# Kernel optimization log

Measured on AMD Instinct MI355X. Metric: run time of the kernel, lower is better.

The kernel has to match this reference:

```python
import jax, jax.numpy as jnp
import numpy as np


def setup_inputs() -> dict:
    key = jax.random.key(0)
    k1, k2, k3 = jax.random.split(key, 3)
    B, Tc, Tq, D = 8, 4096, 1024, 256
    context = jax.random.normal(k1, (B, Tc, D), dtype=jnp.float32)
    question = jax.random.normal(k2, (B, Tq, D), dtype=jnp.float32)
    w = jax.random.normal(k3, (3 * D, 1), dtype=jnp.float32) * 0.05
    return {"context": context, "question": question, "w": w}


def reference(context, question, w):
    # context: (B, Tc, D); question: (B, Tq, D); w: (3D, 1)
    D = context.shape[-1]
    w1, w2, w3 = w[:D, 0], w[D:2 * D, 0], w[2 * D:, 0]
    # Fused similarity: S[b,i,j] = w1.c_i + w2.q_j + w3.(c_i*q_j)
    # (mathematically identical to the tiled concat + linear score, but
    # avoids materializing the (B,Tc,Tq,3D) tensor)
    s_c = jnp.einsum('bid,d->bi', context, w1)              # (B, Tc)
    s_q = jnp.einsum('bjd,d->bj', question, w2)             # (B, Tq)
    s_cq = jnp.einsum('bid,bjd->bij', context * w3, question)  # (B, Tc, Tq)
    S = s_cq + s_c[:, :, None] + s_q[:, None, :]
    A = jax.nn.softmax(S, axis=-1)                           # (B, Tc, Tq)
    # C2Q attention: U[b,i] = sum_j A[b,i,j] * q_j
    U = jnp.einsum('bij,bjd->bid', A, question)              # (B, Tc, D)
    # Q2C attention: b_i = max_j A[b,i,j]; h = sum_i b_i * c_i, tiled over Tc
    b = jnp.max(A, axis=-1)                                  # (B, Tc)
    h = jnp.einsum('bi,bid->bd', b, context)                 # (B, D)
    H = jnp.broadcast_to(h[:, None, :], context.shape)       # (B, Tc, D)
    # megamerge
    G = jnp.concatenate([context, U, context * U, context * H], axis=-1)
    return G  # (B, Tc, 4D)
```

## Files before the change

kernel.cpp:

```cpp
#include <hip/hip_runtime.h>
#include <hip/hip_bf16.h>
#include <stdint.h>
#include <stddef.h>


#define NB 8
#define TC 4096
#define TQ 1024
#define DD 256
#define JT 32
#define NJT (TQ / JT)

typedef __attribute__((ext_vector_type(4)))  float  f32x4v;
typedef __attribute__((ext_vector_type(8)))  __bf16 bf16x8v;
typedef __attribute__((ext_vector_type(4)))  __bf16 bf16x4v;

#define QA_OFF   0
#define QX_OFF   (QA_OFF + NB*NJT*16*1024)
#define SQ_OFF   (QX_OFF + NB*NJT*16*1024)
#define HV_OFF   (SQ_OFF + NB*TQ*4)

__global__ __launch_bounds__(256) void k_qprep(const float* __restrict__ question,
                                               const float* __restrict__ w,
                                               char* __restrict__ ws) {
  uint4* qa = (uint4*)(ws + QA_OFF);
  uint4* qx = (uint4*)(ws + QX_OFF);
  float* sq = (float*)(ws + SQ_OFF);
  __shared__ __align__(16) __bf16 T[32][264];

  int bx = blockIdx.x;
  int b = bx >> 5, it = bx & 31;
  int t = threadIdx.x;
  int j = t >> 3;
  int seg = t & 7;

  const float* qrow = question + ((size_t)(b * TQ + it * JT + j)) * DD + seg * 32;
  const float* w2 = w + DD;

  float part = 0.f;
#pragma unroll
  for (int k = 0; k < 8; ++k) {
    float4 v  = *(const float4*)(qrow + 4 * k);
    float4 wv = *(const float4*)(w2 + seg * 32 + 4 * k);
    part += v.x * wv.x + v.y * wv.y + v.z * wv.z + v.w * wv.w;
    bf16x4v pk = {(__bf16)v.x, (__bf16)v.y, (__bf16)v.z, (__bf16)v.w};
    *(bf16x4v*)&T[j][seg * 32 + 4 * k] = pk;
  }
  part += __shfl_xor(part, 1);
  part += __shfl_xor(part, 2);
  part += __shfl_xor(part, 4);
  if (seg == 0) sq[b * TQ + it * JT + j] = part;
  __syncthreads();

#pragma unroll
  for (int p = 0; p < 4; ++p) {
    int ch = t + 256 * p;
    int L = ch & 63, cc = ch >> 6;
    int jm = cc >> 3, c = cc & 7;
    int nh = L & 15, qh = L >> 4;
    uint4 v = *(const uint4*)&T[16 * jm + nh][32 * c + 8 * qh];
    qa[(size_t)(b * NJT + it) * 1024 + ch] = v;
  }
#pragma unroll
  for (int p = 0; p < 4; ++p) {
    int ch = t + 256 * p;
    int L = ch & 63, mt = ch >> 6;
    int nh = L & 15, qh = L >> 4;
    __bf16 e[8];
#pragma unroll
    for (int o = 0; o < 8; ++o) e[o] = T[8 * qh + o][16 * mt + nh];
    qx[(size_t)(b * NJT + it) * 1024 + ch] = *(const uint4*)e;
  }
}

__global__ __launch_bounds__(256, 2) void k_main(const float* __restrict__ context,
                                                 const float* __restrict__ w,
                                                 const char* __restrict__ ws,
                                                 float* __restrict__ hv,
                                                 float* __restrict__ out) {
  const uint4*  qa = (const uint4*)(ws + QA_OFF);
  const __bf16* qx = (const __bf16*)(ws + QX_OFF);
  const float*  sq = (const float*)(ws + SQ_OFF);

  __shared__ __align__(16) __bf16 pa_lds[2][4][16][40];
  __shared__ __align__(16) float  sq_all[TQ];
  __shared__ __align__(16) float  red_lm[2][4][16][2];
  __shared__ __align__(16) float  rinv_lds[64];
  __shared__ __align__(16) float  bvv_lds[64];

  int bx = blockIdx.x;
  int b = bx & 7;
  int ig = bx >> 3;
  int t = threadIdx.x;
  int wv = t >> 6;
  int lane = t & 63;
  int wi = wv >> 1;
  int wj = wv & 1;
  int it0 = 2 * wi, it1 = 2 * wi + 1;
  int nh = lane & 15;
  int qh = lane >> 4;

  const uint4* qa_b = qa + (size_t)b * NJT * 1024;
  const __bf16* qx_b = qx + (size_t)b * NJT * 8192;
  const float* sqb = sq + b * TQ;

  const uint4* qa_w = qa_b + (size_t)wj * 512 + lane;

  bf16x8v cw3f0[8], cw3f1[8];
  {
    const float* crow0 = context + ((size_t)(b * TC + ig * 64 + 32 * wi + nh)) * DD;
    const float* crow1 = crow0 + 16 * DD;
    const float* w3 = w + 2 * DD;
#pragma unroll
    for (int c = 0; c < 8; ++c) {
      int d0 = 32 * c + 8 * qh;
      float4 g0 = *(const float4*)(w3 + d0);
      float4 g1 = *(const float4*)(w3 + d0 + 4);
      float4 f0 = *(const float4*)(crow0 + d0);
      float4 f1 = *(const float4*)(crow0 + d0 + 4);
      bf16x8v fr;
      fr[0] = (__bf16)(f0.x * g0.x); fr[1] = (__bf16)(f0.y * g0.y);
      fr[2] = (__bf16)(f0.z * g0.z); fr[3] = (__bf16)(f0.w * g0.w);
      fr[4] = (__bf16)(f1.x * g1.x); fr[5] = (__bf16)(f1.y * g1.y);
      fr[6] = (__bf16)(f1.z * g1.z); fr[7] = (__bf16)(f1.w * g1.w);
      cw3f0[c] = fr;
      float4 h0 = *(const float4*)(crow1 + d0);
      float4 h1 = *(const float4*)(crow1 + d0 + 4);
      bf16x8v hr;
      hr[0] = (__bf16)(h0.x * g0.x); hr[1] = (__bf16)(h0.y * g0.y);
      hr[2] = (__bf16)(h0.z * g0.z); hr[3] = (__bf16)(h0.w * g0.w);
      hr[4] = (__bf16)(h1.x * g1.x); hr[5] = (__bf16)(h1.y * g1.y);
      hr[6] = (__bf16)(h1.z * g1.z); hr[7] = (__bf16)(h1.w * g1.w);
      cw3f1[c] = hr;
    }
  }

  ((float4*)sq_all)[t] = ((const float4*)sqb)[t];

  bf16x8v afr[8];
#pragma unroll
  for (int c = 0; c < 8; ++c) afr[c] = *(const bf16x8v*)(qa_w + c * 64);

  f32x4v U[16];
#pragma unroll
  for (int k = 0; k < 16; ++k) U[k] = (f32x4v){0.f, 0.f, 0.f, 0.f};
  float m0_run = -1e30f, l0_run = 0.f;
  float m1_run = -1e30f, l1_run = 0.f;

  __syncthreads();

  {
    f32x4v S0 = {0.f, 0.f, 0.f, 0.f}, S1 = {0.f, 0.f, 0.f, 0.f};
#pragma unroll
    for (int c = 0; c < 8; ++c) {
      S0 = __builtin_amdgcn_mfma_f32_16x16x32_bf16(afr[c], cw3f0[c], S0, 0, 0, 0);
      S1 = __builtin_amdgcn_mfma_f32_16x16x32_bf16(afr[c], cw3f1[c], S1, 0, 0, 0);
    }
#pragma unroll
    for (int c = 0; c < 8; ++c) afr[c] = *(const bf16x8v*)(qa_w + 1024 + c * 64);

    float4 sqv = *(const float4*)&sq_all[16 * wj + 4 * qh];
    float a0 = S0[0] + sqv.x, a1 = S0[1] + sqv.y, a2 = S0[2] + sqv.z, a3 = S0[3] + sqv.w;
    float b0 = S1[0] + sqv.x, b1 = S1[1] + sqv.y, b2 = S1[2] + sqv.z, b3 = S1[3] + sqv.w;
    float e0 = __expf(a0), e1 = __expf(a1), e2 = __expf(a2), e3 = __expf(a3);
    float f0 = __expf(b0), f1 = __expf(b1), f2 = __expf(b2), f3 = __expf(b3);
    m0_run = fmaxf(m0_run, fmaxf(fmaxf(a0, a1), fmaxf(a2, a3)));
    m1_run = fmaxf(m1_run, fmaxf(fmaxf(b0, b1), fmaxf(b2, b3)));
    l0_run += (e0 + e1) + (e2 + e3);
    l1_run += (f0 + f1) + (f2 + f3);
    bf16x4v pk0 = {(__bf16)e0, (__bf16)e1, (__bf16)e2, (__bf16)e3};
    bf16x4v pk1 = {(__bf16)f0, (__bf16)f1, (__bf16)f2, (__bf16)f3};
    *(bf16x4v*)&pa_lds[0][it0][nh][16 * wj + 4 * qh] = pk0;
    *(bf16x4v*)&pa_lds[0][it1][nh][16 * wj + 4 * qh] = pk1;
    asm volatile("s_waitcnt lgkmcnt(0)\n\ts_barrier" ::: "memory");
  }

  for (int itq = 1; itq < NJT; ++itq) {
    int cur = itq & 1;

    bf16x8v bqr[4];
    {
      const __bf16* qxt = qx_b + (size_t)(itq - 1) * 8192 + lane * 8;
#pragma unroll
      for (int nt = 0; nt < 4; ++nt)
        bqr[nt] = *(const bf16x8v*)(qxt + (size_t)(wv * 4 + nt) * 512);
    }

    f32x4v S0 = {0.f, 0.f, 0.f, 0.f}, S1 = {0.f, 0.f, 0.f, 0.f};
#pragma unroll
    for (int c = 0; c < 8; ++c) {
      S0 = __builtin_amdgcn_mfma_f32_16x16x32_bf16(afr[c], cw3f0[c], S0, 0, 0, 0);
      S1 = __builtin_amdgcn_mfma_f32_16x16x32_bf16(afr[c], cw3f1[c], S1, 0, 0, 0);
    }

    if (itq + 1 < NJT) {
#pragma unroll
      for (int c = 0; c < 8; ++c)
        afr[c] = *(const bf16x8v*)(qa_w + (size_t)(itq + 1) * 1024 + c * 64);
    }

#pragma unroll
    for (int mi = 0; mi < 4; ++mi) {
      bf16x8v af = *(const bf16x8v*)&pa_lds[cur ^ 1][mi][nh][8 * qh];
#pragma unroll
      for (int nt = 0; nt < 4; ++nt)
        U[mi * 4 + nt] = __builtin_amdgcn_mfma_f32_16x16x32_bf16(af, bqr[nt], U[mi * 4 + nt], 0, 0, 0);
    }

    float4 sqv = *(const float4*)&sq_all[itq * JT + 16 * wj + 4 * qh];
    float a0 = S0[0] + sqv.x, a1 = S0[1] + sqv.y, a2 = S0[2] + sqv.z, a3 = S0[3] + sqv.w;
    float b0 = S1[0] + sqv.x, b1 = S1[1] + sqv.y, b2 = S1[2] + sqv.z, b3 = S1[3] + sqv.w;
    float e0 = __expf(a0), e1 = __expf(a1), e2 = __expf(a2), e3 = __expf(a3);
    float f0 = __expf(b0), f1 = __expf(b1), f2 = __expf(b2), f3 = __expf(b3);
    m0_run = fmaxf(m0_run, fmaxf(fmaxf(a0, a1), fmaxf(a2, a3)));
    m1_run = fmaxf(m1_run, fmaxf(fmaxf(b0, b1), fmaxf(b2, b3)));
    l0_run += (e0 + e1) + (e2 + e3);
    l1_run += (f0 + f1) + (f2 + f3);

    bf16x4v pk0 = {(__bf16)e0, (__bf16)e1, (__bf16)e2, (__bf16)e3};
    bf16x4v pk1 = {(__bf16)f0, (__bf16)f1, (__bf16)f2, (__bf16)f3};
    *(bf16x4v*)&pa_lds[cur][it0][nh][16 * wj + 4 * qh] = pk0;
    *(bf16x4v*)&pa_lds[cur][it1][nh][16 * wj + 4 * qh] = pk1;

    asm volatile("s_waitcnt lgkmcnt(0)\n\ts_barrier" ::: "memory");
  }

  {
    bf16x8v bqr[4];
    const __bf16* qxt = qx_b + (size_t)(NJT - 1) * 8192 + lane * 8;
#pragma unroll
    for (int nt = 0; nt < 4; ++nt)
      bqr[nt] = *(const bf16x8v*)(qxt + (size_t)(wv * 4 + nt) * 512);
#pragma unroll
    for (int mi = 0; mi < 4; ++mi) {
      bf16x8v af = *(const bf16x8v*)&pa_lds[(NJT - 1) & 1][mi][nh][8 * qh];
#pragma unroll
      for (int nt = 0; nt < 4; ++nt)
        U[mi * 4 + nt] = __builtin_amdgcn_mfma_f32_16x16x32_bf16(af, bqr[nt], U[mi * 4 + nt], 0, 0, 0);
    }
  }

  float lo0 = l0_run + __shfl_xor(l0_run, 16); lo0 += __shfl_xor(lo0, 32);
  float lo1 = l1_run + __shfl_xor(l1_run, 16); lo1 += __shfl_xor(lo1, 32);
  float mo0 = fmaxf(m0_run, __shfl_xor(m0_run, 16)); mo0 = fmaxf(mo0, __shfl_xor(mo0, 32));
  float mo1 = fmaxf(m1_run, __shfl_xor(m1_run, 16)); mo1 = fmaxf(mo1, __shfl_xor(mo1, 32));
  if (lane < 16) {
    red_lm[wj][it0][nh][0] = lo0; red_lm[wj][it0][nh][1] = mo0;
    red_lm[wj][it1][nh][0] = lo1; red_lm[wj][it1][nh][1] = mo1;
  }
  __syncthreads();
  if (t < 64) {
    int it = t >> 4, n = t & 15;
    float l = red_lm[0][it][n][0] + red_lm[1][it][n][0];
    float m = fmaxf(red_lm[0][it][n][1], red_lm[1][it][n][1]);
    float ri = 1.0f / l;
    rinv_lds[t] = ri;
    bvv_lds[t] = __expf(m) * ri;
  }
  __syncthreads();

  float hacc[4] = {0.f, 0.f, 0.f, 0.f};
#pragma unroll
  for (int mi = 0; mi < 4; ++mi) {
#pragma unroll
    for (int r = 0; r < 4; ++r) {
      int rl = mi * 16 + 4 * qh + r;
      int row = ig * 64 + rl;
      float rv = rinv_lds[rl];
      float bb = bvv_lds[rl];
      const float* crow = context + ((size_t)(b * TC + row)) * DD;
      float* orow = out + ((size_t)(b * TC + row)) * (4 * DD);
#pragma unroll
      for (int nt = 0; nt < 4; ++nt) {
        int d = wv * 64 + nt * 16 + nh;
        float c = crow[d];
        float u = U[mi * 4 + nt][r] * rv;
        orow[d] = c;
        orow[DD + d] = u;
        orow[2 * DD + d] = c * u;
        hacc[nt] += bb * c;
      }
    }
  }
#pragma unroll
  for (int nt = 0; nt < 4; ++nt) {
    float h = hacc[nt] + __shfl_xor(hacc[nt], 16);
    h += __shfl_xor(h, 32);
    if (qh == 0) atomicAdd(&hv[b * DD + wv * 64 + nt * 16 + nh], h);
  }
}

__global__ __launch_bounds__(256) void k_final(const float* __restrict__ context,
                                               const char* __restrict__ ws,
                                               float* __restrict__ out) {
  const float* hv = (const float*)(ws + HV_OFF);
  int gid = blockIdx.x * 256 + threadIdx.x;
  int row = gid >> 6;
  int d = (gid & 63) * 4;
  int b = row >> 12;
  float4 c4 = ((const float4*)context)[gid];
  float4 h4 = *(const float4*)(hv + b * DD + d);
  float4 r;
  r.x = c4.x * h4.x; r.y = c4.y * h4.y; r.z = c4.z * h4.z; r.w = c4.w * h4.w;
  *(float4*)(out + (size_t)row * TQ + 3 * DD + d) = r;
}

extern "C" void kernel_launch(void* const* d_in, const int* in_sizes, int n_in,
                              void* d_out, int out_size, void* d_ws, size_t ws_size,
                              hipStream_t stream) {
  (void)in_sizes; (void)n_in; (void)out_size; (void)ws_size;
  const float* context  = (const float*)d_in[0];
  const float* question = (const float*)d_in[1];
  const float* w        = (const float*)d_in[2];
  float* out = (float*)d_out;
  char* ws = (char*)d_ws;

  k_qprep<<<NB * NJT, 256, 0, stream>>>(question, w, ws);
  hipMemsetAsync(ws + HV_OFF, 0, NB * DD * sizeof(float), stream);
  k_main<<<NB * (TC / 64), 256, 0, stream>>>(context, w, ws,
                                             (float*)(ws + HV_OFF), out);
  k_final<<<(NB * TC * DD / 4) / 256, 256, 0, stream>>>(context, ws, out);
}
```

Before: 204.1 us.

## Fuse final Q2C broadcast into main kernel via per-batch grid barrier

```diff
diff --git a/kernel.cpp b/kernel.cpp
--- a/kernel.cpp
+++ b/kernel.cpp
@@ -19,6 +19,7 @@
 #define QX_OFF   (QA_OFF + NB*NJT*16*1024)
 #define SQ_OFF   (QX_OFF + NB*NJT*16*1024)
 #define HV_OFF   (SQ_OFF + NB*TQ*4)
+#define CNT_OFF  (HV_OFF + NB*DD*4)
 
 __global__ __launch_bounds__(256) void k_qprep(const float* __restrict__ question,
                                                const float* __restrict__ w,
@@ -31,6 +32,13 @@
   int bx = blockIdx.x;
   int b = bx >> 5, it = bx & 31;
   int t = threadIdx.x;
+
+  if (it == 0) {
+    float* hvz = (float*)(ws + HV_OFF);
+    hvz[b * DD + t] = 0.f;
+    if (t == 0) *(int*)(ws + CNT_OFF + b * 4) = 0;
+  }
+
   int j = t >> 3;
   int seg = t & 7;
 
@@ -77,6 +85,7 @@
                                                  const float* __restrict__ w,
                                                  const char* __restrict__ ws,
                                                  float* __restrict__ hv,
+                                                 int* __restrict__ cnt,
                                                  float* __restrict__ out) {
   const uint4*  qa = (const uint4*)(ws + QA_OFF);
   const __bf16* qx = (const __bf16*)(ws + QX_OFF);
@@ -288,21 +297,35 @@
     h += __shfl_xor(h, 32);
     if (qh == 0) atomicAdd(&hv[b * DD + wv * 64 + nt * 16 + nh], h);
   }
-}
-
-__global__ __launch_bounds__(256) void k_final(const float* __restrict__ context,
-                                               const char* __restrict__ ws,
-                                               float* __restrict__ out) {
-  const float* hv = (const float*)(ws + HV_OFF);
-  int gid = blockIdx.x * 256 + threadIdx.x;
-  int row = gid >> 6;
-  int d = (gid & 63) * 4;
-  int b = row >> 12;
-  float4 c4 = ((const float4*)context)[gid];
-  float4 h4 = *(const float4*)(hv + b * DD + d);
-  float4 r;
-  r.x = c4.x * h4.x; r.y = c4.y * h4.y; r.z = c4.z * h4.z; r.w = c4.w * h4.w;
-  *(float4*)(out + (size_t)row * TQ + 3 * DD + d) = r;
+
+  __syncthreads();
+  if (t == 0) {
+    __hip_atomic_fetch_add(&cnt[b], 1, __ATOMIC_RELEASE, __HIP_MEMORY_SCOPE_AGENT);
+    while (__hip_atomic_load(&cnt[b], __ATOMIC_ACQUIRE, __HIP_MEMORY_SCOPE_AGENT) < 64) {
+      __builtin_amdgcn_s_sleep(2);
+    }
+  }
+  __syncthreads();
+
+  float hvv[4];
+#pragma unroll
+  for (int nt = 0; nt < 4; ++nt)
+    hvv[nt] = __hip_atomic_load(&hv[b * DD + wv * 64 + nt * 16 + nh],
+                                __ATOMIC_RELAXED, __HIP_MEMORY_SCOPE_AGENT);
+#pragma unroll
+  for (int mi = 0; mi < 4; ++mi) {
+#pragma unroll
+    for (int r = 0; r < 4; ++r) {
+      int row = ig * 64 + mi * 16 + 4 * qh + r;
+      const float* crow = context + ((size_t)(b * TC + row)) * DD;
+      float* orow = out + ((size_t)(b * TC + row)) * (4 * DD);
+#pragma unroll
+      for (int nt = 0; nt < 4; ++nt) {
+        int d = wv * 64 + nt * 16 + nh;
+        orow[3 * DD + d] = crow[d] * hvv[nt];
+      }
+    }
+  }
 }
 
 extern "C" void kernel_launch(void* const* d_in, const int* in_sizes, int n_in,
@@ -314,10 +337,9 @@
   const float* w        = (const float*)d_in[2];
   float* out = (float*)d_out;
   char* ws = (char*)d_ws;
+  float* hv = (float*)(ws + HV_OFF);
+  int* cnt = (int*)(ws + CNT_OFF);
 
   k_qprep<<<NB * NJT, 256, 0, stream>>>(question, w, ws);
-  hipMemsetAsync(ws + HV_OFF, 0, NB * DD * sizeof(float), stream);
-  k_main<<<NB * (TC / 64), 256, 0, stream>>>(context, w, ws,
-                                             (float*)(ws + HV_OFF), out);
-  k_final<<<(NB * TC * DD / 4) / 256, 256, 0, stream>>>(context, ws, out);
+  k_main<<<NB * (TC / 64), 256, 0, stream>>>(context, w, ws, hv, cnt, out);
 }
```

Measured after the change: 314.6 us. 54.2% more time.
